# Kernel optimization log

Measured on AMD Instinct MI355X. Metric: run time of the kernel, lower is better.

Reference implementation:

```python
import jax, jax.numpy as jnp
import numpy as np

NG = 8       # GroupNorm groups
EPS = 1e-5   # torch default eps for GroupNorm/BatchNorm
M_AND = 5    # Anderson history size
MAX_ITER = 25
LAM = 1e-4
BETA = 1.0


def conv2d(x, w):
    # x: [B,C,H,W], w: [O,I,3,3], stride 1, SAME padding (pad=1)
    return jax.lax.conv_general_dilated(x, w, (1, 1), 'SAME',
                                        dimension_numbers=('NCHW', 'OIHW', 'NCHW'))


def group_norm(x, g, b):
    B, C, H, W = x.shape
    xg = x.reshape(B, NG, C // NG, H, W)
    mu = xg.mean((2, 3, 4), keepdims=True)
    var = xg.var((2, 3, 4), keepdims=True)
    xn = ((xg - mu) * jax.lax.rsqrt(var + EPS)).reshape(B, C, H, W)
    return xn * g[None, :, None, None] + b[None, :, None, None]


def batch_norm(x, g, b):
    # training-mode BatchNorm2d: batch statistics over (B,H,W)
    mu = x.mean((0, 2, 3), keepdims=True)
    var = x.var((0, 2, 3), keepdims=True)
    return (x - mu) * jax.lax.rsqrt(var + EPS) * g[None, :, None, None] + b[None, :, None, None]


def resnet_f(p, z, x):
    # y = norm1(relu(conv1(z))); out = norm3(relu(z + norm2(x + conv2(y))))
    y = group_norm(jax.nn.relu(conv2d(z, p['conv1_w'])), p['gn1_g'], p['gn1_b'])
    return group_norm(jax.nn.relu(z + group_norm(x + conv2d(y, p['conv2_w']),
                                                 p['gn2_g'], p['gn2_b'])),
                      p['gn3_g'], p['gn3_b'])


def anderson(f, x0, m=M_AND, lam=LAM, max_iter=MAX_ITER, beta=BETA):
    # Anderson acceleration for fixed point z = f(z); fixed iteration count
    # (the torch version early-exits at tol=0.01; we run the full max_iter for
    # a deterministic jit-friendly reference).
    shape = x0.shape
    bsz = shape[0]
    flat = lambda v: v.reshape(bsz, -1)
    X = [None] * m
    Fv = [None] * m
    X[0] = flat(x0)
    Fv[0] = flat(f(x0))
    X[1] = Fv[0]
    Fv[1] = flat(f(Fv[0].reshape(shape)))
    for k in range(2, max_iter):
        n = min(k, m)
        Xn = jnp.stack(X[:n], 1)   # [B,n,D]
        Fn = jnp.stack(Fv[:n], 1)  # [B,n,D]
        G = Fn - Xn
        Hm = jnp.einsum('bnd,bmd->bnm', G, G) + lam * jnp.eye(n, dtype=x0.dtype)
        Hb = (jnp.zeros((bsz, n + 1, n + 1), x0.dtype)
              .at[:, 1:, 1:].set(Hm)
              .at[:, 0, 1:].set(1.0)
              .at[:, 1:, 0].set(1.0))
        y = jnp.zeros((bsz, n + 1), x0.dtype).at[:, 0].set(1.0)
        alpha = jnp.linalg.solve(Hb, y[..., None])[:, 1:, 0]  # [B,n]
        xk = beta * jnp.einsum('bn,bnd->bd', alpha, Fn) + (1.0 - beta) * jnp.einsum('bn,bnd->bd', alpha, Xn)
        X[k % m] = xk
        Fv[k % m] = flat(f(xk.reshape(shape)))
    return X[(max_iter - 1) % m].reshape(shape)


def setup_inputs() -> dict:
    key = jax.random.key(0)
    ks = jax.random.split(key, 6)
    B, H, W = 8, 128, 200
    f32 = jnp.float32
    return {
        'x': jax.random.normal(ks[0], (B, 1, H, W), f32),
        'conv0_w': jax.random.normal(ks[1], (48, 1, 3, 3), f32) * 0.1,
        'conv0_b': jnp.zeros((48,), f32),
        'bn_g': jnp.ones((48,), f32),
        'bn_b': jnp.zeros((48,), f32),
        'conv1_w': jax.random.normal(ks[2], (64, 48, 3, 3), f32) * 0.01,
        'conv2_w': jax.random.normal(ks[3], (48, 64, 3, 3), f32) * 0.01,
        'gn1_g': jnp.ones((64,), f32), 'gn1_b': jnp.zeros((64,), f32),
        'gn2_g': jnp.ones((48,), f32), 'gn2_b': jnp.zeros((48,), f32),
        'gn3_g': jnp.ones((48,), f32), 'gn3_b': jnp.zeros((48,), f32),
        'fc_w': jax.random.normal(ks[4], (10, 200), f32) * 0.05,
        'fc_b': jnp.zeros((10,), f32),
    }


def reference(x, conv0_w, conv0_b, bn_g, bn_b, conv1_w, conv2_w,
              gn1_g, gn1_b, gn2_g, gn2_b, gn3_g, gn3_b, fc_w, fc_b):
    fp = {'conv1_w': conv1_w, 'conv2_w': conv2_w,
          'gn1_g': gn1_g, 'gn1_b': gn1_b,
          'gn2_g': gn2_g, 'gn2_b': gn2_b,
          'gn3_g': gn3_g, 'gn3_b': gn3_b}
    h = batch_norm(conv2d(x, conv0_w) + conv0_b[None, :, None, None], bn_g, bn_b)
    z_star = anderson(lambda z: resnet_f(fp, z, h), jnp.zeros_like(h))
    z = resnet_f(fp, z_star, h)  # one extra application, as in DEQFixedPoint
    # Linear(200,10) acts on last dim: [B,48,H,200] -> [B,48,H,10]
    return jnp.einsum('bchw,ow->bcho', z, fc_w) + fc_b
```

## Files before the change

kernel.cpp:

```cpp
#include <hip/hip_runtime.h>

#define BB   8
#define HH   128
#define WW   200
#define HWSZ 25600
#define C48  48
#define C64  64
#define NGRP 8
#define EPSV 1e-5f
#define LAMV 1e-4
#define SLOT 9830400
#define DPB  1228800
#define Y64SZ 13107200
#define BIGELEMS 131072000ull

typedef unsigned short bf16_t;
typedef __attribute__((ext_vector_type(4))) short s4v;
typedef __attribute__((ext_vector_type(8))) short s8v;
typedef __attribute__((ext_vector_type(16))) float f32x16;

__device__ inline float b2f(bf16_t b) { return __uint_as_float(((unsigned)b) << 16); }
__device__ inline bf16_t f2b(float f) {
    unsigned u = __float_as_uint(f);
    unsigned r = u + 0x7fffu + ((u >> 16) & 1u);
    return (bf16_t)(r >> 16);
}
__device__ inline float lo16(unsigned u) { return __uint_as_float(u << 16); }
__device__ inline float hi16(unsigned u) { return __uint_as_float(u & 0xffff0000u); }
__device__ inline unsigned pack2(float lo, float hi) {
    return ((unsigned)f2b(lo)) | (((unsigned)f2b(hi)) << 16);
}
__device__ inline float4 ld4(const bf16_t* p) {
    ushort4 u = *(const ushort4*)p;
    return make_float4(b2f(u.x), b2f(u.y), b2f(u.z), b2f(u.w));
}
__device__ inline void st4(bf16_t* p, float4 v) {
    ushort4 u; u.x = f2b(v.x); u.y = f2b(v.y); u.z = f2b(v.z); u.w = f2b(v.w);
    *(ushort4*)p = u;
}
__device__ inline void ld8(const bf16_t* p, float* v) {
    uint4 u = *(const uint4*)p;
    v[0] = lo16(u.x); v[1] = hi16(u.x); v[2] = lo16(u.y); v[3] = hi16(u.y);
    v[4] = lo16(u.z); v[5] = hi16(u.z); v[6] = lo16(u.w); v[7] = hi16(u.w);
}
__device__ inline void st8(bf16_t* p, const float* v) {
    uint4 u;
    u.x = pack2(v[0], v[1]); u.y = pack2(v[2], v[3]);
    u.z = pack2(v[4], v[5]); u.w = pack2(v[6], v[7]);
    *(uint4*)p = u;
}

__device__ inline void ms_from(const double* __restrict__ ds, int pair, double invcnt,
                               float& mean, float& inv) {
    double s = ds[2 * pair], q = ds[2 * pair + 1];
    double m = s * invcnt;
    double v = q * invcnt - m * m;
    mean = (float)m;
    inv = (float)(1.0 / sqrt(v + (double)EPSV));
}


__global__ void zero_kernel(float* __restrict__ p, int n) {
    int i = blockIdx.x * 256 + threadIdx.x;
    if (i < n) p[i] = 0.f;
}
__global__ void fill16_kernel(float4* __restrict__ p) {
    float4 z; z.x = z.y = z.z = z.w = 0.f;
    p[(size_t)blockIdx.x * 256 + threadIdx.x] = z;
}

__global__ void pack_kernel(const float* __restrict__ w, bf16_t* __restrict__ apk,
                            int CIN, int CO_real, int total) {
    int idx = blockIdx.x * 256 + threadIdx.x;
    if (idx >= total) return;
    int j   = idx & 7;
    int l   = (idx >> 3) & 63;
    int mt  = (idx >> 9) & 1;
    int tap = (idx >> 10) % 9;
    int kc  = idx / 9216;
    int co = mt * 32 + (l & 31);
    int ci = kc * 16 + (l >> 5) * 8 + j;
    float v = (co < CO_real) ? w[((size_t)co * CIN + ci) * 9 + tap] : 0.f;
    apk[idx] = f2b(v);
}

__global__ __launch_bounds__(256) void conv0_kernel(
    const float* __restrict__ x, const float* __restrict__ w0,
    const float* __restrict__ b0, float* __restrict__ out,
    double* __restrict__ bnbin)
{
    __shared__ float xs[3 * 202];
    __shared__ float wt[480];
    __shared__ float ss[48], qq[48];
    const int tid = threadIdx.x;
    const int bI = blockIdx.x / HH, y = blockIdx.x % HH;
    for (int i = tid; i < 606; i += 256) {
        int r = i / 202, cc = i % 202;
        int gy = y + r - 1, gx = cc - 1;
        float v = 0.f;
        if ((unsigned)gy < (unsigned)HH && (unsigned)gx < (unsigned)WW)
            v = x[(size_t)bI * HWSZ + gy * WW + gx];
        xs[r * 202 + cc] = v;
    }
    for (int i = tid; i < 480; i += 256) wt[i] = (i < 432) ? w0[i] : b0[i - 432];
    if (tid < 48) { ss[tid] = 0.f; qq[tid] = 0.f; }
    __syncthreads();
    const size_t obase = (((size_t)bI * HH + y) * WW) * 48;
    float4 sacc[3], qacc[3];
    #pragma unroll
    for (int j = 0; j < 3; j++) {
        sacc[j] = make_float4(0.f, 0.f, 0.f, 0.f);
        qacc[j] = make_float4(0.f, 0.f, 0.f, 0.f);
    }
    int k3 = 0;
    for (int ch = tid; ch < 2400; ch += 256) {
        int px = (ch * 4) / 48, c0 = (ch * 4) % 48;
        float xv[3][3];
        #pragma unroll
        for (int r = 0; r < 3; r++)
            #pragma unroll
            for (int dx = 0; dx < 3; dx++)
                xv[r][dx] = xs[r * 202 + px + dx];
        float4 o;
        #pragma unroll
        for (int j = 0; j < 4; j++) {
            int c = c0 + j;
            float acc = wt[432 + c];
            #pragma unroll
            for (int r = 0; r < 3; r++)
                #pragma unroll
                for (int dx = 0; dx < 3; dx++)
                    acc = fmaf(xv[r][dx], wt[c * 9 + r * 3 + dx], acc);
            ((float*)&o)[j] = acc;
        }
        *(float4*)(out + obase + ch * 4) = o;
        sacc[k3].x += o.x; sacc[k3].y += o.y; sacc[k3].z += o.z; sacc[k3].w += o.w;
        qacc[k3].x = fmaf(o.x, o.x, qacc[k3].x);
        qacc[k3].y = fmaf(o.y, o.y, qacc[k3].y);
        qacc[k3].z = fmaf(o.z, o.z, qacc[k3].z);
        qacc[k3].w = fmaf(o.w, o.w, qacc[k3].w);
        k3 = (k3 == 2) ? 0 : k3 + 1;
    }
    #pragma unroll
    for (int j = 0; j < 3; j++) {
        int quad = (tid + 4 * j) % 12;
        atomicAdd(&ss[quad * 4 + 0], sacc[j].x);
        atomicAdd(&ss[quad * 4 + 1], sacc[j].y);
        atomicAdd(&ss[quad * 4 + 2], sacc[j].z);
        atomicAdd(&ss[quad * 4 + 3], sacc[j].w);
        atomicAdd(&qq[quad * 4 + 0], qacc[j].x);
        atomicAdd(&qq[quad * 4 + 1], qacc[j].y);
        atomicAdd(&qq[quad * 4 + 2], qacc[j].z);
        atomicAdd(&qq[quad * 4 + 3], qacc[j].w);
    }
    __syncthreads();
    if (tid < 48) {
        int bin = blockIdx.x & 7;
        unsafeAtomicAdd(&bnbin[bin * 96 + tid * 2],     (double)ss[tid]);
        unsafeAtomicAdd(&bnbin[bin * 96 + tid * 2 + 1], (double)qq[tid]);
    }
}

__global__ void bn_reduce_kernel(const double* __restrict__ bnbin, double* __restrict__ dst) {
    int t = threadIdx.x;
    if (t < 96) {
        double s = 0.0;
        #pragma unroll
        for (int j = 0; j < 8; j++) s += bnbin[j * 96 + t];
        dst[t] = s;
    }
}

__global__ __launch_bounds__(256) void bn_apply_kernel(
    const float* __restrict__ src, bf16_t* __restrict__ dst,
    const float* __restrict__ gamma, const float* __restrict__ beta,
    const double* __restrict__ ds)
{
    __shared__ float gaT[48], beT[48];
    int tid = threadIdx.x;
    if (tid < 48) {
        float mean, inv; ms_from(ds, tid, 1.0 / 204800.0, mean, inv);
        float ga = gamma[tid] * inv;
        gaT[tid] = ga; beT[tid] = beta[tid] - mean * ga;
    }
    __syncthreads();
    size_t base = (size_t)blockIdx.x * 1024 + (size_t)tid * 4;
    int c0 = (int)(base % 48);
    float4 v = *(const float4*)(src + base);
    ushort4 o;
    o.x = f2b(fmaf(v.x, gaT[c0],     beT[c0]));
    o.y = f2b(fmaf(v.y, gaT[c0 + 1], beT[c0 + 1]));
    o.z = f2b(fmaf(v.z, gaT[c0 + 2], beT[c0 + 2]));
    o.w = f2b(fmaf(v.w, gaT[c0 + 3], beT[c0 + 3]));
    *(ushort4*)(dst + base) = o;
}

template<int CIN, int CIPAD, int CO, int OTS, int CG, bool RELU, bool ADDH, bool FOLDGN>
__global__ __launch_bounds__(512, 4) void conv_mfma_kernel(
    const bf16_t* __restrict__ in, const s8v* __restrict__ apk,
    const bf16_t* __restrict__ hadd, bf16_t* __restrict__ out,
    double* __restrict__ dsOut,
    const double* __restrict__ dsPrev, const float* __restrict__ gPrev,
    const float* __restrict__ bPrev)
{
    constexpr int KC  = CIN / 16;
    constexpr int NC8 = CIN / 8;
    constexpr int NITEMS = 10 * 34 * NC8;
    constexpr int NIT = (NITEMS + 511) / 512;
    const int tid  = threadIdx.x;
    const int lane = tid & 63;
    const int wv   = tid >> 6;
    const int x0 = blockIdx.x * 32;
    const int y0 = blockIdx.y * 8;
    const int b  = blockIdx.z;

    __shared__ __align__(16) bf16_t bt[10 * 34 * CIPAD];
    __shared__ __align__(16) s8v ws[1152];
    __shared__ __align__(16) float gaT[FOLDGN ? CIN : 4];
    __shared__ __align__(16) float beT[FOLDGN ? CIN : 4];
    __shared__ float ss[512], qq[512];

    if (FOLDGN) {
        if (tid < CIN) {
            float mean, inv;
            ms_from(dsPrev, b * NGRP + tid / (CIN / NGRP), 1.0 / 204800.0, mean, inv);
            float ga = gPrev[tid] * inv;
            gaT[tid] = ga; beT[tid] = bPrev[tid] - mean * ga;
        }
        __syncthreads();
    }

    s8v vreg[NIT];
    #pragma unroll
    for (int k = 0; k < NIT; k++) {
        int i = tid + k * 512;
        s8v t;
        #pragma unroll
        for (int e = 0; e < 8; e++) t[e] = 0;
        if (i < NITEMS) {
            int ch8 = i % NC8, p = i / NC8;
            int r = p / 34, c = p - r * 34;
            int gy = y0 + r - 1, gx = x0 + c - 1;
            if ((unsigned)gy < (unsigned)HH && (unsigned)gx < (unsigned)WW)
                t = *(const s8v*)(in + ((((size_t)b * HH + gy) * WW + gx) * CIN + ch8 * 8));
        }
        vreg[k] = t;
    }
    #pragma unroll
    for (int k = 0; k < NIT; k++) {
        int i = tid + k * 512;
        if (i >= NITEMS) continue;
        int ch8 = i % NC8, p = i / NC8;
        s8v v = vreg[k];
        if (FOLDGN) {
            int r = p / 34, c = p - r * 34;
            int gy = y0 + r - 1, gx = x0 + c - 1;
            if ((unsigned)gy < (unsigned)HH && (unsigned)gx < (unsigned)WW) {
                const float* ga8 = &gaT[ch8 * 8];
                const float* be8 = &beT[ch8 * 8];
                float f[8];
                #pragma unroll
                for (int e = 0; e < 8; e++)
                    f[e] = fmaf(b2f((bf16_t)(unsigned short)v[e]), ga8[e], be8[e]);
                unsigned p01, p23, p45, p67;
                asm("v_cvt_pk_bf16_f32 %0, %1, %2" : "=v"(p01) : "v"(f[0]), "v"(f[1]));
                asm("v_cvt_pk_bf16_f32 %0, %1, %2" : "=v"(p23) : "v"(f[2]), "v"(f[3]));
                asm("v_cvt_pk_bf16_f32 %0, %1, %2" : "=v"(p45) : "v"(f[4]), "v"(f[5]));
                asm("v_cvt_pk_bf16_f32 %0, %1, %2" : "=v"(p67) : "v"(f[6]), "v"(f[7]));
                unsigned* vp = (unsigned*)&v;
                vp[0] = p01; vp[1] = p23; vp[2] = p45; vp[3] = p67;
            }
        }
        *(s8v*)(bt + p * CIPAD + ch8 * 8) = v;
    }

    const int n = lane & 31, half = lane >> 5;
    f32x16 acc0, acc1;
    #pragma unroll
    for (int i = 0; i < 16; i++) { acc0[i] = 0.f; acc1[i] = 0.f; }

    #pragma unroll
    for (int kc = 0; kc < KC; kc++) {
        if (kc) __syncthreads();
        for (int i = tid; i < 1152; i += 512)
            ws[i] = apk[(size_t)kc * 1152 + i];
        __syncthreads();
        #pragma unroll
        for (int ky = 0; ky < 3; ky++)
        #pragma unroll
        for (int kx = 0; kx < 3; kx++) {
            const int tap = ky * 3 + kx;
            s8v a0 = ws[tap * 128 + lane];
            s8v a1 = ws[tap * 128 + 64 + lane];
            const bf16_t* brow = bt + ((wv + ky) * 34 + n + kx) * CIPAD + half * 8;
            s8v bfrag = *(const s8v*)(brow + kc * 16);
            acc0 = __builtin_amdgcn_mfma_f32_32x32x16_bf16(a0, bfrag, acc0, 0, 0, 0);
            acc1 = __builtin_amdgcn_mfma_f32_32x32x16_bf16(a1, bfrag, acc1, 0, 0, 0);
        }
    }
    __syncthreads();

    bf16_t* ot = bt;
    {
        const int pxl = wv * 32 + n;
        const bool pv = (x0 + n) < WW;
        #pragma unroll
        for (int g4 = 0; g4 < 4; g4++) {
            s4v pk0;
            #pragma unroll
            for (int jj = 0; jj < 4; jj++) {
                float v = acc0[g4 * 4 + jj];
                if (RELU) v = fmaxf(v, 0.f);
                pk0[jj] = (short)(pv ? f2b(v) : (bf16_t)0);
            }
            *(s4v*)&ot[pxl * OTS + g4 * 8 + 4 * half] = pk0;
            const int c1b = 32 + g4 * 8 + 4 * half;
            if (c1b + 3 < CO) {
                s4v pk1;
                #pragma unroll
                for (int jj = 0; jj < 4; jj++) {
                    float v = acc1[g4 * 4 + jj];
                    if (RELU) v = fmaxf(v, 0.f);
                    pk1[jj] = (short)(pv ? f2b(v) : (bf16_t)0);
                }
                *(s4v*)&ot[pxl * OTS + c1b] = pk1;
            }
        }
    }
    __syncthreads();
    {
        constexpr int NCH8 = 256 * CO / 8;
        for (int ch = tid; ch < NCH8; ch += 512) {
            int pxl = ch / (CO / 8);
            int co0 = (ch % (CO / 8)) * 8;
            int row = pxl >> 5, col = pxl & 31;
            int xx = x0 + col;
            if (xx < WW) {
                bf16_t* lp = &ot[pxl * OTS + co0];
                size_t ga = (((size_t)b * HH + y0 + row) * WW + xx) * CO + co0;
                if (ADDH) {
                    float4 h0 = ld4(hadd + ga), h1 = ld4(hadd + ga + 4);
                    float4 l0 = ld4(lp), l1 = ld4(lp + 4);
                    float4 v0 = make_float4(l0.x + h0.x, l0.y + h0.y, l0.z + h0.z, l0.w + h0.w);
                    float4 v1 = make_float4(l1.x + h1.x, l1.y + h1.y, l1.z + h1.z, l1.w + h1.w);
                    st4(out + ga, v0); st4(out + ga + 4, v1);
                    st4(lp, v0); st4(lp + 4, v1);
                } else {
                    *(ushort4*)(out + ga)     = *(ushort4*)lp;
                    *(ushort4*)(out + ga + 4) = *(ushort4*)(lp + 4);
                }
            }
        }
    }
    if (ADDH) __syncthreads();
    {
        constexpr int NPH = 512 / CO;
        const int c = tid % CO, rr = tid / CO;
        float s = 0.f, q = 0.f;
        if (rr < NPH) {
            for (int px = rr; px < 256; px += NPH) {
                float v = b2f(ot[px * OTS + c]);
                s += v; q += v * v;
            }
        }
        ss[tid] = s; qq[tid] = q;
        __syncthreads();
        if (tid < CO) {
            float S = ss[tid], Q = qq[tid];
            #pragma unroll
            for (int p = 1; p < NPH; p++) { S += ss[tid + p * CO]; Q += qq[tid + p * CO]; }
            ss[tid] = S; qq[tid] = Q;
        }
        __syncthreads();
        if (tid < NGRP) {
            float S = 0.f, Q = 0.f;
            #pragma unroll
            for (int j = 0; j < CG; j++) { S += ss[tid * CG + j]; Q += qq[tid * CG + j]; }
            unsafeAtomicAdd(&dsOut[((size_t)b * NGRP + tid) * 2],     (double)S);
            unsafeAtomicAdd(&dsOut[((size_t)b * NGRP + tid) * 2 + 1], (double)Q);
        }
    }
}

__global__ __launch_bounds__(192) void add_relu_gn2_kernel(
    bf16_t* __restrict__ u, const bf16_t* __restrict__ z,
    const double* __restrict__ ds2, const float* __restrict__ g2,
    const float* __restrict__ b2, double* __restrict__ ds3)
{
    __shared__ float sm[16];
    const int tid = threadIdx.x;
    const int c0 = 8 * (tid % 6), pxr = tid / 6;
    const int b = blockIdx.y;
    if (tid < 16) sm[tid] = 0.f;
    const int gA = c0 / 6;
    const int split = (gA + 1) * 6 - c0;
    float meanA, invA, meanB, invB;
    ms_from(ds2, b * NGRP + gA,     1.0 / 153600.0, meanA, invA);
    ms_from(ds2, b * NGRP + gA + 1, 1.0 / 153600.0, meanB, invB);
    float wga[8], wbe[8];
    #pragma unroll
    for (int e = 0; e < 8; e++) {
        int c = c0 + e;
        float m = (e < split) ? meanA : meanB, iv = (e < split) ? invA : invB;
        float ga = g2[c] * iv;
        wga[e] = ga; wbe[e] = b2[c] - m * ga;
    }
    __syncthreads();
    const size_t pxbase = (size_t)b * HWSZ + (size_t)blockIdx.x * 256;
    float sA = 0.f, qA = 0.f, sB = 0.f, qB = 0.f;
    for (int it = 0; it < 8; it++) {
        size_t idx = (pxbase + it * 32 + pxr) * 48 + c0;
        float uu[8], zz[8], vv[8];
        ld8(u + idx, uu); ld8(z + idx, zz);
        #pragma unroll
        for (int e = 0; e < 8; e++) {
            float v = fmaxf(fmaf(uu[e], wga[e], wbe[e]) + zz[e], 0.f);
            vv[e] = v;
            if (e < split) { sA += v; qA += v * v; } else { sB += v; qB += v * v; }
        }
        st8(u + idx, vv);
    }
    atomicAdd(&sm[2 * gA], sA);     atomicAdd(&sm[2 * gA + 1], qA);
    atomicAdd(&sm[2 * gA + 2], sB); atomicAdd(&sm[2 * gA + 3], qB);
    __syncthreads();
    if (tid < NGRP) {
        unsafeAtomicAdd(&ds3[(b * NGRP + tid) * 2],     (double)sm[tid * 2]);
        unsafeAtomicAdd(&ds3[(b * NGRP + tid) * 2 + 1], (double)sm[tid * 2 + 1]);
    }
}

__global__ __launch_bounds__(192) void gn3_gram_kernel(
    const bf16_t* __restrict__ v, const bf16_t* __restrict__ z,
    bf16_t* __restrict__ F, bf16_t* __restrict__ G,
    const double* __restrict__ ds3, const float* __restrict__ g3,
    const float* __restrict__ b3,
    const bf16_t* __restrict__ Gall, int jslot, int nf, double* __restrict__ gram)
{
    __shared__ double red[3][5];
    const int tid = threadIdx.x;
    const int c0 = 8 * (tid % 6), pxr = tid / 6;
    const int b = blockIdx.y;
    const int gA = c0 / 6;
    const int split = (gA + 1) * 6 - c0;
    float meanA, invA, meanB, invB;
    ms_from(ds3, b * NGRP + gA,     1.0 / 153600.0, meanA, invA);
    ms_from(ds3, b * NGRP + gA + 1, 1.0 / 153600.0, meanB, invB);
    float wga[8], wbe[8];
    #pragma unroll
    for (int e = 0; e < 8; e++) {
        int c = c0 + e;
        float m = (e < split) ? meanA : meanB, iv = (e < split) ? invA : invB;
        float ga = g3[c] * iv;
        wga[e] = ga; wbe[e] = b3[c] - m * ga;
    }
    const size_t pxbase = (size_t)b * HWSZ + (size_t)blockIdx.x * 256;
    double dot[5] = {0.0, 0.0, 0.0, 0.0, 0.0};
    for (int it = 0; it < 8; it++) {
        size_t idx = (pxbase + it * 32 + pxr) * 48 + c0;
        float rr[8];
        ld8(v + idx, rr);
        #pragma unroll
        for (int e = 0; e < 8; e++) rr[e] = fmaf(rr[e], wga[e], wbe[e]);
        st8(F + idx, rr);
        if (nf > 0) {
            float zz[8], gg[8];
            ld8(z + idx, zz);
            #pragma unroll
            for (int e = 0; e < 8; e++) gg[e] = rr[e] - zz[e];
            st8(G + idx, gg);
            #pragma unroll
            for (int i = 0; i < 5; i++) {
                if (i >= nf) continue;
                float d = 0.f;
                if (i == jslot) {
                    #pragma unroll
                    for (int e = 0; e < 8; e++) d = fmaf(gg[e], gg[e], d);
                } else {
                    float gi[8];
                    ld8(Gall + (size_t)i * SLOT + idx, gi);
                    #pragma unroll
                    for (int e = 0; e < 8; e++) d = fmaf(gg[e], gi[e], d);
                }
                dot[i] += (double)d;
            }
        }
    }
    if (nf > 0) {
        #pragma unroll
        for (int i = 0; i < 5; i++) {
            if (i >= nf) continue;
            #pragma unroll
            for (int off = 32; off > 0; off >>= 1) dot[i] += __shfl_down(dot[i], off);
        }
        int wv = tid >> 6;
        if ((tid & 63) == 0) {
            #pragma unroll
            for (int i = 0; i < 5; i++) if (i < nf) red[wv][i] = dot[i];
        }
        __syncthreads();
        if (tid == 0) {
            #pragma unroll
            for (int i = 0; i < 5; i++) {
                if (i >= nf) continue;
                double D = red[0][i] + red[1][i] + red[2][i];
                unsafeAtomicAdd(&gram[b * 25 + jslot * 5 + i], D);
                if (i != jslot) unsafeAtomicAdd(&gram[b * 25 + i * 5 + jslot], D);
            }
        }
    }
}

__global__ void solve_kernel(const double* __restrict__ gram, float* __restrict__ alpha, int n) {
    int b = threadIdx.x;
    if (b >= BB) return;
    const int m = n + 1;
    double A[6][7];
    for (int i = 0; i < m; i++)
        for (int jj = 0; jj <= m; jj++) A[i][jj] = 0.0;
    for (int i = 1; i < m; i++) { A[0][i] = 1.0; A[i][0] = 1.0; }
    for (int i = 1; i < m; i++)
        for (int jj = 1; jj < m; jj++)
            A[i][jj] = gram[b * 25 + (i - 1) * 5 + (jj - 1)] + ((i == jj) ? LAMV : 0.0);
    A[0][m] = 1.0;
    for (int col = 0; col < m; col++) {
        int piv = col; double best = fabs(A[col][col]);
        for (int rr = col + 1; rr < m; rr++) {
            double tv = fabs(A[rr][col]);
            if (tv > best) { best = tv; piv = rr; }
        }
        if (piv != col)
            for (int cc = col; cc <= m; cc++) {
                double tmp = A[col][cc]; A[col][cc] = A[piv][cc]; A[piv][cc] = tmp;
            }
        double invp = 1.0 / A[col][col];
        for (int cc = col; cc <= m; cc++) A[col][cc] *= invp;
        for (int rr = 0; rr < m; rr++) {
            if (rr == col) continue;
            double f = A[rr][col];
            if (f != 0.0)
                for (int cc = col; cc <= m; cc++) A[rr][cc] = fma(-f, A[col][cc], A[rr][cc]);
        }
    }
    for (int i = 0; i < n; i++) alpha[b * 5 + i] = (float)A[i + 1][m];
}

__global__ __launch_bounds__(256) void xk_kernel(
    const bf16_t* __restrict__ Fb, const float* __restrict__ alpha,
    bf16_t* __restrict__ zcur, int n, double* __restrict__ gram, int jz, int nf)
{
    if (blockIdx.x == 0 && threadIdx.x < 8 * nf) {
        int b = threadIdx.x / nf, i = threadIdx.x % nf;
        gram[b * 25 + jz * 5 + i] = 0.0;
        gram[b * 25 + i * 5 + jz] = 0.0;
    }
    const int b = blockIdx.x / 300;
    float al[5];
    #pragma unroll
    for (int j = 0; j < 5; j++) al[j] = (j < n) ? alpha[b * 5 + j] : 0.f;
    const size_t base = (size_t)blockIdx.x * 4096 + (size_t)threadIdx.x * 8;
    for (int it = 0; it < 2; it++) {
        size_t idx = base + (size_t)it * 2048;
        float s[8] = {0.f, 0.f, 0.f, 0.f, 0.f, 0.f, 0.f, 0.f};
        #pragma unroll
        for (int j = 0; j < 5; j++) {
            if (j < n) {
                float f[8];
                ld8(Fb + (size_t)j * SLOT + idx, f);
                #pragma unroll
                for (int e = 0; e < 8; e++) s[e] = fmaf(f[e], al[j], s[e]);
            }
        }
        st8(zcur + idx, s);
    }
}

__global__ __launch_bounds__(512) void fc_kernel(
    const bf16_t* __restrict__ zf, const float* __restrict__ fw,
    const float* __restrict__ fb, float* __restrict__ out)
{
    __shared__ bf16_t row[9600];
    __shared__ float fwT[2000];
    int tid = threadIdx.x;
    int b = blockIdx.x >> 7, hh = blockIdx.x & 127;
    size_t base = (((size_t)b * HH + hh) * WW) * 48;
    for (int i = tid; i < 2400; i += 512)
        *(ushort4*)&row[i * 4] = *(const ushort4*)(zf + base + (size_t)i * 4);
    for (int i = tid; i < 2000; i += 512) fwT[i] = fw[i];
    __syncthreads();
    if (tid < 480) {
        int c = tid % 48, o = tid / 48;
        float acc = fb[o];
        #pragma unroll 4
        for (int w = 0; w < 200; w++)
            acc = fmaf(b2f(row[w * 48 + c]), fwT[o * 200 + w], acc);
        out[(((size_t)b * 48 + c) * HH + hh) * 10 + o] = acc;
    }
}


static inline int imin(int a, int b) { return a < b ? a : b; }

extern "C" void kernel_launch(void* const* d_in, const int* in_sizes, int n_in,
                              void* d_out, int out_size, void* d_ws, size_t ws_size,
                              hipStream_t stream)
{
    const float* x   = (const float*)d_in[0];
    const float* w0  = (const float*)d_in[1];
    const float* b0  = (const float*)d_in[2];
    const float* bng = (const float*)d_in[3];
    const float* bnb = (const float*)d_in[4];
    const float* w1  = (const float*)d_in[5];
    const float* w2  = (const float*)d_in[6];
    const float* g1  = (const float*)d_in[7];
    const float* be1 = (const float*)d_in[8];
    const float* g2  = (const float*)d_in[9];
    const float* be2 = (const float*)d_in[10];
    const float* g3  = (const float*)d_in[11];
    const float* be3 = (const float*)d_in[12];
    const float* fcw = (const float*)d_in[13];
    const float* fcb = (const float*)d_in[14];
    float* out = (float*)d_out;

    bf16_t* h    = (bf16_t*)d_ws;
    bf16_t* zcur = h + (size_t)SLOT;
    bf16_t* y64  = zcur + (size_t)SLOT;
    bf16_t* Fb   = y64 + (size_t)Y64SZ;
    bf16_t* Gb   = Fb + 5 * (size_t)SLOT;
    double* dstats = (double*)((char*)d_ws + BIGELEMS * 2);
    double* gram   = dstats + 9696;
    float*  alpha  = (float*)(gram + 200);
    double* bnbin  = (double*)(alpha + 40);
    bf16_t* apk1   = (bf16_t*)(bnbin + 768);
    bf16_t* apk2   = apk1 + 27648;
    float*  scratch = (float*)Gb;

    const size_t need = BIGELEMS * 2 + 9696 * 8 + 200 * 8 + 40 * 4 + 768 * 8
                        + (27648 + 36864) * 2;
    if (ws_size < need) return;

    const dim3 blk(256);
    const int CHUNKS16 = SLOT * 2 / 16 / 256;

    zero_kernel<<<(21368 + 255) / 256, blk, 0, stream>>>((float*)dstats, 21368);
    pack_kernel<<<108, blk, 0, stream>>>(w1, apk1, 48, 64, 27648);
    pack_kernel<<<144, blk, 0, stream>>>(w2, apk2, 64, 48, 36864);
    fill16_kernel<<<CHUNKS16, blk, 0, stream>>>((float4*)zcur);

    conv0_kernel<<<BB * HH, blk, 0, stream>>>(x, w0, b0, scratch, bnbin);
    bn_reduce_kernel<<<1, 128, 0, stream>>>(bnbin, dstats);
    bn_apply_kernel<<<SLOT / 1024, blk, 0, stream>>>(scratch, h, bng, bnb, dstats);

    int call = 0;
    auto resnet = [&](const bf16_t* zin, bf16_t* Fdst, bf16_t* Gdst, int jslot, int nf) {
        double* ds = dstats + 96 + 384 * call;
        call++;
        dim3 cgv(7, 16, BB);
        conv_mfma_kernel<48, 56, 64, 66, 8, true, false, false><<<cgv, dim3(512), 0, stream>>>(
            zin, (const s8v*)apk1, nullptr, y64, ds, nullptr, nullptr, nullptr);
        conv_mfma_kernel<64, 72, 48, 50, 6, false, true, true><<<cgv, dim3(512), 0, stream>>>(
            y64, (const s8v*)apk2, h, Fdst, ds + 128, ds, g1, be1);
        add_relu_gn2_kernel<<<dim3(100, BB), dim3(192), 0, stream>>>(
            Fdst, zin, ds + 128, g2, be2, ds + 256);
        gn3_gram_kernel<<<dim3(100, BB), dim3(192), 0, stream>>>(
            Fdst, zin, Fdst, Gdst, ds + 256, g3, be3, Gb, jslot, nf, gram);
    };

    resnet(zcur, Fb, Gb, 0, 1);
    resnet(Fb, Fb + (size_t)SLOT, Gb + (size_t)SLOT, 1, 2);

    for (int k = 2; k <= 24; k++) {
        int n = imin(k, 5);
        int j = k % 5;
        int nf = imin(k + 1, 5);
        solve_kernel<<<1, 64, 0, stream>>>(gram, alpha, n);
        xk_kernel<<<2400, blk, 0, stream>>>(Fb, alpha, zcur, n, gram, j, nf);
        if (k < 24)
            resnet(zcur, Fb + (size_t)j * SLOT, Gb + (size_t)j * SLOT, j, nf);
    }

    resnet(zcur, Fb, nullptr, 0, 0);

    fc_kernel<<<BB * HH, dim3(512), 0, stream>>>(Fb, fcw, fcb, out);
}
```

Measured before the change: 4.601 ms.

## Prefetch next weight chunk into registers during MFMA conv; split conv0 rows

```diff
diff --git a/kernel.cpp b/kernel.cpp
--- a/kernel.cpp
+++ b/kernel.cpp
@@ -89,23 +89,25 @@
     const float* __restrict__ b0, float* __restrict__ out,
     double* __restrict__ bnbin)
 {
-    __shared__ float xs[3 * 202];
+    __shared__ float xs[3 * 102];
     __shared__ float wt[480];
     __shared__ float ss[48], qq[48];
     const int tid = threadIdx.x;
-    const int bI = blockIdx.x / HH, y = blockIdx.x % HH;
-    for (int i = tid; i < 606; i += 256) {
-        int r = i / 202, cc = i % 202;
-        int gy = y + r - 1, gx = cc - 1;
+    const int bI = blockIdx.x / (HH * 2);
+    const int rem = blockIdx.x % (HH * 2);
+    const int y = rem >> 1, xoff = (rem & 1) * 100;
+    for (int i = tid; i < 306; i += 256) {
+        int r = i / 102, cc = i % 102;
+        int gy = y + r - 1, gx = xoff + cc - 1;
         float v = 0.f;
         if ((unsigned)gy < (unsigned)HH && (unsigned)gx < (unsigned)WW)
             v = x[(size_t)bI * HWSZ + gy * WW + gx];
-        xs[r * 202 + cc] = v;
+        xs[r * 102 + cc] = v;
     }
     for (int i = tid; i < 480; i += 256) wt[i] = (i < 432) ? w0[i] : b0[i - 432];
     if (tid < 48) { ss[tid] = 0.f; qq[tid] = 0.f; }
     __syncthreads();
-    const size_t obase = (((size_t)bI * HH + y) * WW) * 48;
+    const size_t obase = (((size_t)bI * HH + y) * WW + xoff) * 48;
     float4 sacc[3], qacc[3];
     #pragma unroll
     for (int j = 0; j < 3; j++) {
@@ -113,14 +115,14 @@
         qacc[j] = make_float4(0.f, 0.f, 0.f, 0.f);
     }
     int k3 = 0;
-    for (int ch = tid; ch < 2400; ch += 256) {
+    for (int ch = tid; ch < 1200; ch += 256) {
         int px = (ch * 4) / 48, c0 = (ch * 4) % 48;
         float xv[3][3];
         #pragma unroll
         for (int r = 0; r < 3; r++)
             #pragma unroll
             for (int dx = 0; dx < 3; dx++)
-                xv[r][dx] = xs[r * 202 + px + dx];
+                xv[r][dx] = xs[r * 102 + px + dx];
         float4 o;
         #pragma unroll
         for (int j = 0; j < 4; j++) {
@@ -246,6 +248,11 @@
         }
         vreg[k] = t;
     }
+    s8v wr0 = apk[tid];
+    s8v wr1 = apk[tid + 512];
+    s8v wr2;
+    if (tid < 128) wr2 = apk[tid + 1024];
+
     #pragma unroll
     for (int k = 0; k < NIT; k++) {
         int i = tid + k * 512;
@@ -273,6 +280,10 @@
         }
         *(s8v*)(bt + p * CIPAD + ch8 * 8) = v;
     }
+    ws[tid] = wr0;
+    ws[tid + 512] = wr1;
+    if (tid < 128) ws[tid + 1024] = wr2;
+    __syncthreads();
 
     const int n = lane & 31, half = lane >> 5;
     f32x16 acc0, acc1;
@@ -281,10 +292,12 @@
 
     #pragma unroll
     for (int kc = 0; kc < KC; kc++) {
-        if (kc) __syncthreads();
-        for (int i = tid; i < 1152; i += 512)
-            ws[i] = apk[(size_t)kc * 1152 + i];
-        __syncthreads();
+        if (kc + 1 < KC) {
+            const s8v* anext = apk + (size_t)(kc + 1) * 1152;
+            wr0 = anext[tid];
+            wr1 = anext[tid + 512];
+            if (tid < 128) wr2 = anext[tid + 1024];
+        }
         #pragma unroll
         for (int ky = 0; ky < 3; ky++)
         #pragma unroll
@@ -296,6 +309,13 @@
             s8v bfrag = *(const s8v*)(brow + kc * 16);
             acc0 = __builtin_amdgcn_mfma_f32_32x32x16_bf16(a0, bfrag, acc0, 0, 0, 0);
             acc1 = __builtin_amdgcn_mfma_f32_32x32x16_bf16(a1, bfrag, acc1, 0, 0, 0);
+        }
+        if (kc + 1 < KC) {
+            __syncthreads();
+            ws[tid] = wr0;
+            ws[tid + 512] = wr1;
+            if (tid < 128) ws[tid + 1024] = wr2;
+            __syncthreads();
         }
     }
     __syncthreads();
@@ -646,7 +666,7 @@
     pack_kernel<<<144, blk, 0, stream>>>(w2, apk2, 64, 48, 36864);
     fill16_kernel<<<CHUNKS16, blk, 0, stream>>>((float4*)zcur);
 
-    conv0_kernel<<<BB * HH, blk, 0, stream>>>(x, w0, b0, scratch, bnbin);
+    conv0_kernel<<<BB * HH * 2, blk, 0, stream>>>(x, w0, b0, scratch, bnbin);
     bn_reduce_kernel<<<1, 128, 0, stream>>>(bnbin, dstats);
     bn_apply_kernel<<<SLOT / 1024, blk, 0, stream>>>(scratch, h, bng, bnb, dstats);
 
```

Measured after the change: 4.667 ms. About the same (+1.5%).

## Fuse Anderson mixing step into first conv's input load

Applied to the files above, without the earlier changes.

```diff
diff --git a/kernel.cpp b/kernel.cpp
--- a/kernel.cpp
+++ b/kernel.cpp
@@ -195,13 +195,16 @@
     *(ushort4*)(dst + base) = o;
 }
 
-template<int CIN, int CIPAD, int CO, int OTS, int CG, bool RELU, bool ADDH, bool FOLDGN>
+template<int CIN, int CIPAD, int CO, int OTS, int CG, bool RELU, bool ADDH, bool FOLDGN,
+         bool FUSEXK>
 __global__ __launch_bounds__(512, 4) void conv_mfma_kernel(
     const bf16_t* __restrict__ in, const s8v* __restrict__ apk,
     const bf16_t* __restrict__ hadd, bf16_t* __restrict__ out,
     double* __restrict__ dsOut,
     const double* __restrict__ dsPrev, const float* __restrict__ gPrev,
-    const float* __restrict__ bPrev)
+    const float* __restrict__ bPrev,
+    const bf16_t* __restrict__ FbX, const float* __restrict__ alphaX,
+    bf16_t* __restrict__ zwr, int nX)
 {
     constexpr int KC  = CIN / 16;
     constexpr int NC8 = CIN / 8;
@@ -230,48 +233,84 @@
         __syncthreads();
     }
 
-    s8v vreg[NIT];
-    #pragma unroll
-    for (int k = 0; k < NIT; k++) {
-        int i = tid + k * 512;
-        s8v t;
-        #pragma unroll
-        for (int e = 0; e < 8; e++) t[e] = 0;
-        if (i < NITEMS) {
+    if (FUSEXK) {
+        float al[5];
+        #pragma unroll
+        for (int j = 0; j < 5; j++) al[j] = (j < nX) ? alphaX[b * 5 + j] : 0.f;
+        for (int k = 0; k < NIT; k++) {
+            int i = tid + k * 512;
+            if (i >= NITEMS) continue;
             int ch8 = i % NC8, p = i / NC8;
             int r = p / 34, c = p - r * 34;
             int gy = y0 + r - 1, gx = x0 + c - 1;
-            if ((unsigned)gy < (unsigned)HH && (unsigned)gx < (unsigned)WW)
-                t = *(const s8v*)(in + ((((size_t)b * HH + gy) * WW + gx) * CIN + ch8 * 8));
-        }
-        vreg[k] = t;
-    }
-    #pragma unroll
-    for (int k = 0; k < NIT; k++) {
-        int i = tid + k * 512;
-        if (i >= NITEMS) continue;
-        int ch8 = i % NC8, p = i / NC8;
-        s8v v = vreg[k];
-        if (FOLDGN) {
-            int r = p / 34, c = p - r * 34;
-            int gy = y0 + r - 1, gx = x0 + c - 1;
+            s8v v;
+            #pragma unroll
+            for (int e = 0; e < 8; e++) v[e] = 0;
             if ((unsigned)gy < (unsigned)HH && (unsigned)gx < (unsigned)WW) {
-                const float* ga8 = &gaT[ch8 * 8];
-                const float* be8 = &beT[ch8 * 8];
-                float f[8];
+                size_t gidx = (((size_t)b * HH + gy) * WW + gx) * CIN + ch8 * 8;
+                float zf[8] = {0.f, 0.f, 0.f, 0.f, 0.f, 0.f, 0.f, 0.f};
                 #pragma unroll
-                for (int e = 0; e < 8; e++)
-                    f[e] = fmaf(b2f((bf16_t)(unsigned short)v[e]), ga8[e], be8[e]);
-                unsigned p01, p23, p45, p67;
-                asm("v_cvt_pk_bf16_f32 %0, %1, %2" : "=v"(p01) : "v"(f[0]), "v"(f[1]));
-                asm("v_cvt_pk_bf16_f32 %0, %1, %2" : "=v"(p23) : "v"(f[2]), "v"(f[3]));
-                asm("v_cvt_pk_bf16_f32 %0, %1, %2" : "=v"(p45) : "v"(f[4]), "v"(f[5]));
-                asm("v_cvt_pk_bf16_f32 %0, %1, %2" : "=v"(p67) : "v"(f[6]), "v"(f[7]));
-                unsigned* vp = (unsigned*)&v;
-                vp[0] = p01; vp[1] = p23; vp[2] = p45; vp[3] = p67;
-            }
-        }
-        *(s8v*)(bt + p * CIPAD + ch8 * 8) = v;
+                for (int j = 0; j < 5; j++) {
+                    if (j < nX) {
+                        float f[8];
+                        ld8(FbX + (size_t)j * SLOT + gidx, f);
+                        #pragma unroll
+                        for (int e = 0; e < 8; e++) zf[e] = fmaf(f[e], al[j], zf[e]);
+                    }
+                }
+                uint4 upk;
+                upk.x = pack2(zf[0], zf[1]); upk.y = pack2(zf[2], zf[3]);
+                upk.z = pack2(zf[4], zf[5]); upk.w = pack2(zf[6], zf[7]);
+                v = *(s8v*)&upk;
+                if (r >= 1 && r <= 8 && c >= 1 && c <= 32)
+                    *(s8v*)(zwr + gidx) = v;
+            }
+            *(s8v*)(bt + p * CIPAD + ch8 * 8) = v;
+        }
+    } else {
+        s8v vreg[NIT];
+        #pragma unroll
+        for (int k = 0; k < NIT; k++) {
+            int i = tid + k * 512;
+            s8v t;
+            #pragma unroll
+            for (int e = 0; e < 8; e++) t[e] = 0;
+            if (i < NITEMS) {
+                int ch8 = i % NC8, p = i / NC8;
+                int r = p / 34, c = p - r * 34;
+                int gy = y0 + r - 1, gx = x0 + c - 1;
+                if ((unsigned)gy < (unsigned)HH && (unsigned)gx < (unsigned)WW)
+                    t = *(const s8v*)(in + ((((size_t)b * HH + gy) * WW + gx) * CIN + ch8 * 8));
+            }
+            vreg[k] = t;
+        }
+        #pragma unroll
+        for (int k = 0; k < NIT; k++) {
+            int i = tid + k * 512;
+            if (i >= NITEMS) continue;
+            int ch8 = i % NC8, p = i / NC8;
+            s8v v = vreg[k];
+            if (FOLDGN) {
+                int r = p / 34, c = p - r * 34;
+                int gy = y0 + r - 1, gx = x0 + c - 1;
+                if ((unsigned)gy < (unsigned)HH && (unsigned)gx < (unsigned)WW) {
+                    const float* ga8 = &gaT[ch8 * 8];
+                    const float* be8 = &beT[ch8 * 8];
+                    float f[8];
+                    #pragma unroll
+                    for (int e = 0; e < 8; e++)
+                        f[e] = fmaf(b2f((bf16_t)(unsigned short)v[e]), ga8[e], be8[e]);
+                    unsigned p01, p23, p45, p67;
+                    asm("v_cvt_pk_bf16_f32 %0, %1, %2" : "=v"(p01) : "v"(f[0]), "v"(f[1]));
+                    asm("v_cvt_pk_bf16_f32 %0, %1, %2" : "=v"(p23) : "v"(f[2]), "v"(f[3]));
+                    asm("v_cvt_pk_bf16_f32 %0, %1, %2" : "=v"(p45) : "v"(f[4]), "v"(f[5]));
+                    asm("v_cvt_pk_bf16_f32 %0, %1, %2" : "=v"(p67) : "v"(f[6]), "v"(f[7]));
+                    unsigned* vp = (unsigned*)&v;
+                    vp[0] = p01; vp[1] = p23; vp[2] = p45; vp[3] = p67;
+                }
+            }
+            *(s8v*)(bt + p * CIPAD + ch8 * 8) = v;
+        }
     }
 
     const int n = lane & 31, half = lane >> 5;
@@ -510,7 +549,8 @@
     }
 }
 
-__global__ void solve_kernel(const double* __restrict__ gram, float* __restrict__ alpha, int n) {
+__global__ void solve_kernel(double* __restrict__ gram, float* __restrict__ alpha,
+                             int n, int jz, int nf) {
     int b = threadIdx.x;
     if (b >= BB) return;
     const int m = n + 1;
@@ -542,35 +582,9 @@
         }
     }
     for (int i = 0; i < n; i++) alpha[b * 5 + i] = (float)A[i + 1][m];
-}
-
-__global__ __launch_bounds__(256) void xk_kernel(
-    const bf16_t* __restrict__ Fb, const float* __restrict__ alpha,
-    bf16_t* __restrict__ zcur, int n, double* __restrict__ gram, int jz, int nf)
-{
-    if (blockIdx.x == 0 && threadIdx.x < 8 * nf) {
-        int b = threadIdx.x / nf, i = threadIdx.x % nf;
+    for (int i = 0; i < nf; i++) {
         gram[b * 25 + jz * 5 + i] = 0.0;
         gram[b * 25 + i * 5 + jz] = 0.0;
-    }
-    const int b = blockIdx.x / 300;
-    float al[5];
-    #pragma unroll
-    for (int j = 0; j < 5; j++) al[j] = (j < n) ? alpha[b * 5 + j] : 0.f;
-    const size_t base = (size_t)blockIdx.x * 4096 + (size_t)threadIdx.x * 8;
-    for (int it = 0; it < 2; it++) {
-        size_t idx = base + (size_t)it * 2048;
-        float s[8] = {0.f, 0.f, 0.f, 0.f, 0.f, 0.f, 0.f, 0.f};
-        #pragma unroll
-        for (int j = 0; j < 5; j++) {
-            if (j < n) {
-                float f[8];
-                ld8(Fb + (size_t)j * SLOT + idx, f);
-                #pragma unroll
-                for (int e = 0; e < 8; e++) s[e] = fmaf(f[e], al[j], s[e]);
-            }
-        }
-        st8(zcur + idx, s);
     }
 }
 
@@ -651,34 +665,46 @@
     bn_apply_kernel<<<SLOT / 1024, blk, 0, stream>>>(scratch, h, bng, bnb, dstats);
 
     int call = 0;
-    auto resnet = [&](const bf16_t* zin, bf16_t* Fdst, bf16_t* Gdst, int jslot, int nf) {
+    auto resnet = [&](const bf16_t* zin, bf16_t* Fdst, bf16_t* Gdst, int jslot, int nf,
+                      bool fused, int nX) {
         double* ds = dstats + 96 + 384 * call;
         call++;
         dim3 cgv(7, 16, BB);
-        conv_mfma_kernel<48, 56, 64, 66, 8, true, false, false><<<cgv, dim3(512), 0, stream>>>(
-            zin, (const s8v*)apk1, nullptr, y64, ds, nullptr, nullptr, nullptr);
-        conv_mfma_kernel<64, 72, 48, 50, 6, false, true, true><<<cgv, dim3(512), 0, stream>>>(
-            y64, (const s8v*)apk2, h, Fdst, ds + 128, ds, g1, be1);
+        if (fused) {
+            conv_mfma_kernel<48, 56, 64, 66, 8, true, false, false, true>
+                <<<cgv, dim3(512), 0, stream>>>(
+                zcur, (const s8v*)apk1, nullptr, y64, ds, nullptr, nullptr, nullptr,
+                Fb, alpha, zcur, nX);
+        } else {
+            conv_mfma_kernel<48, 56, 64, 66, 8, true, false, false, false>
+                <<<cgv, dim3(512), 0, stream>>>(
+                zin, (const s8v*)apk1, nullptr, y64, ds, nullptr, nullptr, nullptr,
+                nullptr, nullptr, nullptr, 0);
+        }
+        conv_mfma_kernel<64, 72, 48, 50, 6, false, true, true, false>
+            <<<cgv, dim3(512), 0, stream>>>(
+            y64, (const s8v*)apk2, h, Fdst, ds + 128, ds, g1, be1,
+            nullptr, nullptr, nullptr, 0);
+        const bf16_t* zread = fused ? zcur : zin;
         add_relu_gn2_kernel<<<dim3(100, BB), dim3(192), 0, stream>>>(
-            Fdst, zin, ds + 128, g2, be2, ds + 256);
+            Fdst, zread, ds + 128, g2, be2, ds + 256);
         gn3_gram_kernel<<<dim3(100, BB), dim3(192), 0, stream>>>(
-            Fdst, zin, Fdst, Gdst, ds + 256, g3, be3, Gb, jslot, nf, gram);
+            Fdst, zread, Fdst, Gdst, ds + 256, g3, be3, Gb, jslot, nf, gram);
     };
 
-    resnet(zcur, Fb, Gb, 0, 1);
-    resnet(Fb, Fb + (size_t)SLOT, Gb + (size_t)SLOT, 1, 2);
+    resnet(zcur, Fb, Gb, 0, 1, false, 0);
+    resnet(Fb, Fb + (size_t)SLOT, Gb + (size_t)SLOT, 1, 2, false, 0);
 
     for (int k = 2; k <= 24; k++) {
         int n = imin(k, 5);
         int j = k % 5;
         int nf = imin(k + 1, 5);
-        solve_kernel<<<1, 64, 0, stream>>>(gram, alpha, n);
-        xk_kernel<<<2400, blk, 0, stream>>>(Fb, alpha, zcur, n, gram, j, nf);
+        solve_kernel<<<1, 64, 0, stream>>>(gram, alpha, n, j, nf);
         if (k < 24)
-            resnet(zcur, Fb + (size_t)j * SLOT, Gb + (size_t)j * SLOT, j, nf);
-    }
-
-    resnet(zcur, Fb, nullptr, 0, 0);
+            resnet(nullptr, Fb + (size_t)j * SLOT, Gb + (size_t)j * SLOT, j, nf, true, n);
+    }
+
+    resnet(nullptr, Fb, nullptr, 0, 0, true, 5);
 
     fc_kernel<<<BB * HH, dim3(512), 0, stream>>>(Fb, fcw, fcb, out);
 }
```

Measured after the change: 4.640 ms. Within noise of the previous version (+0.9%).
